# Kernel tuning notes

Hardware: AMD Instinct MI355X
Metric: run time of the kernel (lower is better)

Reference implementation:

```python
import jax, jax.numpy as jnp
import numpy as np
import math

STD = math.exp(0.0025)  # exp(0.5 * 0.005) from log_sigma = 0.005
C = 0.5 * math.log(2 * math.pi)
B, X, H, Z, L, W = 8192, 512, 256, 64, 16, 32

def _predict(h, Wd, bd, Wo, bo):
    return jax.nn.sigmoid(jax.nn.relu(h @ Wd.T + bd) @ Wo.T + bo)

def _gru(xin, h, Wih, Whh, bih, bhh):
    gi = xin @ Wih.T + bih
    gh = h @ Whh.T + bhh
    ir, iz, inn = jnp.split(gi, 3, axis=1)
    hr, hz, hn = jnp.split(gh, 3, axis=1)
    r = jax.nn.sigmoid(ir + hr)
    zt = jax.nn.sigmoid(iz + hz)
    n = jnp.tanh(inn + r * hn)
    return (1.0 - zt) * n + zt * h

def setup_inputs():
    key = jax.random.key(0)
    ks = iter(jax.random.split(key, 40))
    def nrm(shape, s=0.05):
        return jax.random.normal(next(ks), shape, dtype=jnp.float32) * s
    return {
        "x": jax.random.uniform(next(ks), (B, X), dtype=jnp.float32),
        "workers": jax.random.uniform(next(ks), (W, B, L), dtype=jnp.float32),
        "Wf1": nrm((H, X)), "bf1": jnp.zeros((H,)),
        "Wf2": nrm((1, H)), "bf2": jnp.zeros((1,)),
        "eWih": nrm((L, 3 * H, X + 1)), "eWhh": nrm((L, 3 * H, H)),
        "ebih": jnp.zeros((L, 3 * H)), "ebhh": jnp.zeros((L, 3 * H)),
        "eWd": nrm((L, H, H)), "ebd": jnp.zeros((L, H)),
        "eWo": nrm((L, 1, H)), "ebo": jnp.zeros((L, 1)),
        "Wmu": nrm((Z, H)), "bmu": jnp.zeros((Z,)),
        "Wlv": nrm((Z, H)), "blv": jnp.zeros((Z,)),
        "dWih": nrm((L, 3 * H, Z + 1)), "dWhh": nrm((L, 3 * H, H)),
        "dbih": jnp.zeros((L, 3 * H)), "dbhh": jnp.zeros((L, 3 * H)),
        "dWd": nrm((L, H, H)), "dbd": jnp.zeros((L, H)),
        "dWo": nrm((L, W, H)), "dbo": jnp.zeros((L, W)),
        "Wr": nrm((X, H)), "br": jnp.zeros((X,)),
        "enc_eps": jax.random.normal(next(ks), (L, B, H), dtype=jnp.float32),
        "samp_eps": jax.random.normal(next(ks), (B, Z), dtype=jnp.float32),
        "dec_eps": jax.random.uniform(next(ks), (L, B, H), dtype=jnp.float32),
    }

def _forward(x, workers, Wf1, bf1, Wf2, bf2, eWih, eWhh, ebih, ebhh, eWd, ebd, eWo, ebo,
             Wmu, bmu, Wlv, blv, dWih, dWhh, dbih, dbhh, dWd, dbd, dWo, dbo, Wr, br,
             enc_eps, samp_eps, dec_eps):
    nB = x.shape[0]
    h_dim = eWhh.shape[2]
    # Encoder: t[:,0] = firstcell(x)
    t0 = _predict(x, Wf1, bf1, Wf2, bf2)[:, 0]
    z0 = jnp.zeros((nB, h_dim), dtype=x.dtype)

    def enc_step(carry, xs):
        z, ti = carry
        Wih, Whh, bih, bhh, Wd, bd, Wo, bo, eps = xs
        tmp = (ti >= 0.5).astype(x.dtype)
        mu = _gru(jnp.concatenate([x, tmp[:, None]], axis=1), z, Wih, Whh, bih, bhh)
        znew = mu + STD * eps
        tn = _predict(znew, Wd, bd, Wo, bo)[:, 0]
        return (znew, tn), ti

    (z_fin, _), tcols = jax.lax.scan(
        enc_step, (z0, t0), (eWih, eWhh, ebih, ebhh, eWd, ebd, eWo, ebo, enc_eps))
    t = tcols.T  # [B, L]
    mu_z = z_fin @ Wmu.T + bmu
    log_var = jax.nn.softplus(z_fin @ Wlv.T + blv)
    latent = mu_z + jnp.exp(0.5 * log_var) * samp_eps
    tmp_t = (t > 0.5).astype(x.dtype)

    def dec_step(zt, xs):
        Wih, Whh, bih, bhh, Wd, bd, Wo, bo, tcol, eps = xs
        mu = _gru(jnp.concatenate([latent, tcol[:, None]], axis=1), zt, Wih, Whh, bih, bhh)
        znew = mu + STD * eps  # decoder uses uniform eps (torch.rand)
        return znew, _predict(znew, Wd, bd, Wo, bo)

    zT, preds = jax.lax.scan(
        dec_step, jnp.zeros((nB, h_dim), dtype=x.dtype),
        (dWih, dWhh, dbih, dbhh, dWd, dbd, dWo, dbo, tmp_t.T, dec_eps))
    worker_preds = jnp.transpose(preds, (2, 1, 0))  # [L,B,W] -> [W,B,L]
    recon = jax.nn.sigmoid(zT @ Wr.T + br)
    log_p_x = jnp.sum(x * jnp.log(recon), axis=1)
    logp = jnp.clip(jnp.log(worker_preds), -100.0)
    log1mp = jnp.clip(jnp.log1p(-worker_preds), -100.0)
    bce = -(workers * logp + (1.0 - workers) * log1mp)
    log_p_y = -jnp.sum(jnp.sum(bce, axis=0), axis=1)
    workers_bar = jnp.mean(workers, axis=0)
    log_kl = jnp.sum(t * (jnp.log(t + 1e-6) - jnp.log(workers_bar + 1e-6)), axis=1)
    log_p_z = jnp.sum(-C - latent ** 2 / 2, axis=-1)
    log_q = jnp.sum(-C - log_var / 2 - (latent - mu_z) ** 2 / (2 * jnp.exp(log_var)), axis=-1)
    loss = jnp.mean(log_q - log_p_z - log_p_y - log_p_x + log_kl)
    return t, loss

def reference(x, workers, Wf1, bf1, Wf2, bf2, eWih, eWhh, ebih, ebhh, eWd, ebd, eWo, ebo,
              Wmu, bmu, Wlv, blv, dWih, dWhh, dbih, dbhh, dWd, dbd, dWo, dbo, Wr, br,
              enc_eps, samp_eps, dec_eps):
    return _forward(x, workers, Wf1, bf1, Wf2, bf2, eWih, eWhh, ebih, ebhh, eWd, ebd,
                    eWo, ebo, Wmu, bmu, Wlv, blv, dWih, dWhh, dbih, dbhh, dWd, dbd,
                    dWo, dbo, Wr, br, enc_eps, samp_eps, dec_eps)
```

## Files before the change

kernel.cpp:

```cpp
#include <hip/hip_runtime.h>
#include <hip/hip_bf16.h>
#include <math.h>

#define B_ 8192
#define X_ 512
#define H_ 256
#define Z_ 64
#define L_ 16
#define W_ 32
#define G3_ 768

#define STDF 1.0025031276057952f
#define CC 0.9189385332046727f

typedef _Float16 f16x8 __attribute__((ext_vector_type(8)));
typedef float f32x4 __attribute__((ext_vector_type(4)));

__device__ __forceinline__ float sigm(float x) { return 1.0f / (1.0f + expf(-x)); }
__device__ __forceinline__ float logsig(float u) {
    return (u > 0.0f) ? -log1pf(expf(-u)) : (u - log1pf(expf(u)));
}

#define GLOAD16(gsrc, ldst) \
    __builtin_amdgcn_global_load_lds((const __attribute__((address_space(1))) unsigned int*)(gsrc), \
                                     (__attribute__((address_space(3))) unsigned int*)(ldst), 16, 0, 0)

#define WAITV(N) asm volatile("s_waitcnt vmcnt(" #N ")" ::: "memory")
#define SBAR()  do { __builtin_amdgcn_sched_barrier(0); __builtin_amdgcn_s_barrier(); } while (0)

template<int BN>
__global__ __launch_bounds__(256) void mfma_gemm(
    const _Float16* __restrict__ A,
    const _Float16* __restrict__ Wt,
    const float* __restrict__ bias,
    float* __restrict__ C, int ldc,
    int K, int act)
{
    constexpr int BM = 128;
    constexpr int WN = BN / 2;
    constexpr int NFR = WN / 16;
    __shared__ char smem[2][(BM + BN) * 128];

    const int tid  = threadIdx.x;
    const int wave = tid >> 6;
    const int lane = tid & 63;
    const int wr   = wave >> 1;
    const int wc   = wave & 1;
    const int bm   = blockIdx.y * BM;
    const int bn   = blockIdx.x * BN;
    const int l15  = lane & 15;
    const int l4   = lane >> 4;

    f32x4 acc[4][NFR];
    #pragma unroll
    for (int a = 0; a < 4; ++a)
        #pragma unroll
        for (int b = 0; b < NFR; ++b) {
            f32x4 zz = {0.f, 0.f, 0.f, 0.f};
            acc[a][b] = zz;
        }

    auto stage = [&](int s, int pb) {
        char* As = smem[pb];
        char* Ws = smem[pb] + BM * 128;
        int k0 = s * 64;
        #pragma unroll
        for (int it = 0; it < 4; ++it) {
            int q   = it * 4 + wave;
            int o   = q * 1024 + lane * 16;
            int row = o >> 7;
            int c   = ((o >> 4) & 7) ^ (row & 7);
            GLOAD16(A + (long)(bm + row) * K + k0 + c * 8, As + q * 1024);
        }
        #pragma unroll
        for (int it = 0; it < BN / 32; ++it) {
            int q   = it * 4 + wave;
            int o   = q * 1024 + lane * 16;
            int row = o >> 7;
            int c   = ((o >> 4) & 7) ^ (row & 7);
            GLOAD16(Wt + (long)(bn + row) * K + k0 + c * 8, Ws + q * 1024);
        }
    };

    const int NT = K >> 6;
    stage(0, 0);
    for (int s = 0; s < NT; ++s) {
        int pb = s & 1;
        if (s + 1 < NT) {
            stage(s + 1, pb ^ 1);
            if constexpr (BN == 128) WAITV(8); else WAITV(6);
        } else WAITV(0);
        SBAR();
        char* As = smem[pb];
        char* Ws = smem[pb] + BM * 128;
        #pragma unroll
        for (int ks = 0; ks < 2; ++ks) {
            f16x8 af[4], bf[NFR];
            #pragma unroll
            for (int mi = 0; mi < 4; ++mi) {
                int row = wr * 64 + mi * 16 + l15;
                int c   = (ks * 4 + l4) ^ (row & 7);
                af[mi] = *(const f16x8*)(As + row * 128 + c * 16);
            }
            #pragma unroll
            for (int ni = 0; ni < NFR; ++ni) {
                int row = wc * WN + ni * 16 + l15;
                int c   = (ks * 4 + l4) ^ (row & 7);
                bf[ni] = *(const f16x8*)(Ws + row * 128 + c * 16);
            }
            #pragma unroll
            for (int mi = 0; mi < 4; ++mi)
                #pragma unroll
                for (int ni = 0; ni < NFR; ++ni)
                    acc[mi][ni] = __builtin_amdgcn_mfma_f32_16x16x32_f16(
                        af[mi], bf[ni], acc[mi][ni], 0, 0, 0);
        }
        SBAR();
    }

    #pragma unroll
    for (int mi = 0; mi < 4; ++mi)
        #pragma unroll
        for (int r = 0; r < 4; ++r) {
            int grow = bm + wr * 64 + mi * 16 + l4 * 4 + r;
            #pragma unroll
            for (int ni = 0; ni < NFR; ++ni) {
                int gcol = bn + wc * WN + ni * 16 + l15;
                float v = acc[mi][ni][r] + bias[gcol];
                if (act) v = fmaxf(v, 0.0f);
                C[(long)grow * ldc + gcol] = v;
            }
        }
}

template<int MODE, int KX, int FIRST>
__global__ __launch_bounds__(256) void gru_fused(
    const _Float16* __restrict__ A2,
    const _Float16* __restrict__ Wih,
    const float* __restrict__ bih,
    const _Float16* __restrict__ Whh,
    const float* __restrict__ bhh,
    const float* __restrict__ ec,
    const float* __restrict__ tcol,
    const float* __restrict__ eps,
    const _Float16* __restrict__ zh_in,
    float* __restrict__ z,
    _Float16* __restrict__ zh_out)
{
    constexpr int N1 = KX / 64;
    constexpr int NT = N1 + (FIRST ? 0 : 4);
    __shared__ char smem[2][(64 + 192) * 128];

    const int tid  = threadIdx.x;
    const int wave = tid >> 6;
    const int lane = tid & 63;
    const int wr   = wave >> 1;
    const int wc   = wave & 1;
    const int id   = blockIdx.x;
    const int xcd  = id & 7;
    const int wk   = id >> 3;
    const int bm   = (xcd * 16 + (wk >> 2)) * 64;
    const int h0   = (wk & 3) * 64;
    const int l15  = lane & 15;
    const int l4   = lane >> 4;

    f32x4 acc[2][6];
    f32x4 accN[2][2];
    #pragma unroll
    for (int a = 0; a < 2; ++a) {
        #pragma unroll
        for (int b = 0; b < 6; ++b) { f32x4 zz = {0.f,0.f,0.f,0.f}; acc[a][b] = zz; }
        #pragma unroll
        for (int b = 0; b < 2; ++b) { f32x4 zz = {0.f,0.f,0.f,0.f}; accN[a][b] = zz; }
    }

    auto stage = [&](int s, int pb) {
        char* As = smem[pb];
        char* Ws = smem[pb] + 64 * 128;
        const _Float16* srcA;
        const _Float16* srcW;
        int KA, k0;
        if (s < N1) { srcA = A2;    srcW = Wih; KA = KX;  k0 = s * 64; }
        else        { srcA = zh_in; srcW = Whh; KA = 256; k0 = (s - N1) * 64; }
        #pragma unroll
        for (int it = 0; it < 2; ++it) {
            int q   = it * 4 + wave;
            int o   = q * 1024 + lane * 16;
            int row = o >> 7;
            int c   = ((o >> 4) & 7) ^ (row & 7);
            GLOAD16(srcA + (long)(bm + row) * KA + k0 + c * 8, As + q * 1024);
        }
        #pragma unroll
        for (int it = 0; it < 6; ++it) {
            int q   = it * 4 + wave;
            int o   = q * 1024 + lane * 16;
            int rr  = o >> 7;
            int c   = ((o >> 4) & 7) ^ (rr & 7);
            int srow = (rr >> 6) * 256 + h0 + (rr & 63);
            GLOAD16(srcW + (long)srow * KA + k0 + c * 8, Ws + q * 1024);
        }
    };

    stage(0, 0);
    for (int s = 0; s < NT; ++s) {
        int pb = s & 1;
        if (s + 1 < NT) { stage(s + 1, pb ^ 1); WAITV(8); }
        else WAITV(0);
        SBAR();
        char* As = smem[pb];
        char* Ws = smem[pb] + 64 * 128;
        bool p1 = (s < N1);
        #pragma unroll
        for (int ks = 0; ks < 2; ++ks) {
            f16x8 af[2], bf[6];
            #pragma unroll
            for (int mi = 0; mi < 2; ++mi) {
                int row = wr * 32 + mi * 16 + l15;
                int c   = (ks * 4 + l4) ^ (row & 7);
                af[mi] = *(const f16x8*)(As + row * 128 + c * 16);
            }
            #pragma unroll
            for (int ni = 0; ni < 6; ++ni) {
                int rr = (ni >> 1) * 64 + wc * 32 + (ni & 1) * 16 + l15;
                int c  = (ks * 4 + l4) ^ (rr & 7);
                bf[ni] = *(const f16x8*)(Ws + rr * 128 + c * 16);
            }
            if (p1) {
                #pragma unroll
                for (int mi = 0; mi < 2; ++mi) {
                    #pragma unroll
                    for (int ni = 0; ni < 4; ++ni)
                        acc[mi][ni] = __builtin_amdgcn_mfma_f32_16x16x32_f16(
                            af[mi], bf[ni], acc[mi][ni], 0, 0, 0);
                    #pragma unroll
                    for (int ni = 4; ni < 6; ++ni)
                        accN[mi][ni - 4] = __builtin_amdgcn_mfma_f32_16x16x32_f16(
                            af[mi], bf[ni], accN[mi][ni - 4], 0, 0, 0);
                }
            } else {
                #pragma unroll
                for (int mi = 0; mi < 2; ++mi)
                    #pragma unroll
                    for (int ni = 0; ni < 6; ++ni)
                        acc[mi][ni] = __builtin_amdgcn_mfma_f32_16x16x32_f16(
                            af[mi], bf[ni], acc[mi][ni], 0, 0, 0);
            }
        }
        SBAR();
    }

    #pragma unroll
    for (int mi = 0; mi < 2; ++mi)
        #pragma unroll
        for (int r = 0; r < 4; ++r) {
            int grow = bm + wr * 32 + mi * 16 + l4 * 4 + r;
            float tv = tcol[(long)grow * L_];
            float ext = (MODE == 1) ? (tv >= 0.5f ? 1.0f : 0.0f)
                                    : (tv >  0.5f ? 1.0f : 0.0f);
            #pragma unroll
            for (int hb = 0; hb < 2; ++hb) {
                int h = h0 + wc * 32 + hb * 16 + l15;
                float rpre = acc[mi][hb][r]     + bih[h]       + bhh[h]       + ext * ec[h];
                float zpre = acc[mi][2 + hb][r] + bih[256 + h] + bhh[256 + h] + ext * ec[256 + h];
                float hn   = acc[mi][4 + hb][r] + bhh[512 + h];
                float in_  = accN[mi][hb][r]    + bih[512 + h] + ext * ec[512 + h];
                float rg = sigm(rpre);
                float zt = sigm(zpre);
                float n  = tanhf(in_ + rg * hn);
                long zi = (long)grow * 256 + h;
                float zold = FIRST ? 0.0f : z[zi];
                float v = (1.0f - zt) * n + zt * zold + STDF * eps[zi];
                z[zi] = v;
                zh_out[zi] = (_Float16)v;
            }
        }
}

template<int K>
__global__ __launch_bounds__(256) void predict_head(
    const _Float16* __restrict__ A,
    const _Float16* __restrict__ Wd,
    const float* __restrict__ bd,
    const float* __restrict__ wo,
    const float* __restrict__ bo,
    float* __restrict__ out, int ostride)
{
    constexpr int NT = K / 64;
    __shared__ char smem[2][(32 + 256) * 128];
    __shared__ float part[32][4];

    const int tid  = threadIdx.x;
    const int wave = tid >> 6;
    const int lane = tid & 63;
    const int bm   = blockIdx.x * 32;
    const int l15  = lane & 15;
    const int l4   = lane >> 4;

    f32x4 acc[2][4];
    #pragma unroll
    for (int a = 0; a < 2; ++a)
        #pragma unroll
        for (int b = 0; b < 4; ++b) { f32x4 zz = {0.f,0.f,0.f,0.f}; acc[a][b] = zz; }

    auto stage = [&](int s, int pb) {
        char* As = smem[pb];
        char* Ws = smem[pb] + 32 * 128;
        int k0 = s * 64;
        {
            int o   = wave * 1024 + lane * 16;
            int row = o >> 7;
            int c   = ((o >> 4) & 7) ^ (row & 7);
            GLOAD16(A + (long)(bm + row) * K + k0 + c * 8, As + wave * 1024);
        }
        #pragma unroll
        for (int it = 0; it < 8; ++it) {
            int q   = it * 4 + wave;
            int o   = q * 1024 + lane * 16;
            int row = o >> 7;
            int c   = ((o >> 4) & 7) ^ (row & 7);
            GLOAD16(Wd + (long)row * K + k0 + c * 8, Ws + q * 1024);
        }
    };

    stage(0, 0);
    for (int s = 0; s < NT; ++s) {
        int pb = s & 1;
        if (s + 1 < NT) { stage(s + 1, pb ^ 1); WAITV(9); }
        else WAITV(0);
        SBAR();
        char* As = smem[pb];
        char* Ws = smem[pb] + 32 * 128;
        #pragma unroll
        for (int ks = 0; ks < 2; ++ks) {
            f16x8 af[2], bf[4];
            #pragma unroll
            for (int mi = 0; mi < 2; ++mi) {
                int row = mi * 16 + l15;
                int c   = (ks * 4 + l4) ^ (row & 7);
                af[mi] = *(const f16x8*)(As + row * 128 + c * 16);
            }
            #pragma unroll
            for (int ni = 0; ni < 4; ++ni) {
                int row = wave * 64 + ni * 16 + l15;
                int c   = (ks * 4 + l4) ^ (row & 7);
                bf[ni] = *(const f16x8*)(Ws + row * 128 + c * 16);
            }
            #pragma unroll
            for (int mi = 0; mi < 2; ++mi)
                #pragma unroll
                for (int ni = 0; ni < 4; ++ni)
                    acc[mi][ni] = __builtin_amdgcn_mfma_f32_16x16x32_f16(
                        af[mi], bf[ni], acc[mi][ni], 0, 0, 0);
        }
        SBAR();
    }

    float bdv[4], wov[4];
    #pragma unroll
    for (int ni = 0; ni < 4; ++ni) {
        int col = wave * 64 + ni * 16 + l15;
        bdv[ni] = bd[col];
        wov[ni] = wo[col];
    }
    #pragma unroll
    for (int mi = 0; mi < 2; ++mi)
        #pragma unroll
        for (int r = 0; r < 4; ++r) {
            float s = 0.0f;
            #pragma unroll
            for (int ni = 0; ni < 4; ++ni) {
                float v = fmaxf(acc[mi][ni][r] + bdv[ni], 0.0f);
                s = fmaf(v, wov[ni], s);
            }
            #pragma unroll
            for (int off = 1; off < 16; off <<= 1) s += __shfl_xor(s, off, 16);
            if (l15 == 0) part[mi * 16 + l4 * 4 + r][wave] = s;
        }
    __syncthreads();
    if (tid < 32) {
        float u = part[tid][0] + part[tid][1] + part[tid][2] + part[tid][3] + bo[0];
        out[(long)(bm + tid) * ostride] = sigm(u);
    }
}

__global__ __launch_bounds__(256) void dec_head_bce(
    const _Float16* __restrict__ A,
    const _Float16* __restrict__ Wd,
    const float* __restrict__ bd,
    const _Float16* __restrict__ Wo,
    const float* __restrict__ bo,
    const float* __restrict__ wt,
    float* __restrict__ bacc)
{
    constexpr int NT = 4;
    __shared__ char smem[2][(32 + 256) * 128];
    __shared__ _Float16 ds[32 * 264];
    __shared__ float part[32][2];

    const int tid  = threadIdx.x;
    const int wave = tid >> 6;
    const int lane = tid & 63;
    const int bm   = blockIdx.x * 32;
    const int l15  = lane & 15;
    const int l4   = lane >> 4;

    f32x4 acc[2][4];
    #pragma unroll
    for (int a = 0; a < 2; ++a)
        #pragma unroll
        for (int b = 0; b < 4; ++b) { f32x4 zz = {0.f,0.f,0.f,0.f}; acc[a][b] = zz; }

    auto stage = [&](int s, int pb) {
        char* As = smem[pb];
        char* Ws = smem[pb] + 32 * 128;
        int k0 = s * 64;
        {
            int o   = wave * 1024 + lane * 16;
            int row = o >> 7;
            int c   = ((o >> 4) & 7) ^ (row & 7);
            GLOAD16(A + (long)(bm + row) * 256 + k0 + c * 8, As + wave * 1024);
        }
        #pragma unroll
        for (int it = 0; it < 8; ++it) {
            int q   = it * 4 + wave;
            int o   = q * 1024 + lane * 16;
            int row = o >> 7;
            int c   = ((o >> 4) & 7) ^ (row & 7);
            GLOAD16(Wd + (long)row * 256 + k0 + c * 8, Ws + q * 1024);
        }
    };

    stage(0, 0);
    for (int s = 0; s < NT; ++s) {
        int pb = s & 1;
        if (s + 1 < NT) { stage(s + 1, pb ^ 1); WAITV(9); }
        else WAITV(0);
        SBAR();
        char* As = smem[pb];
        char* Ws = smem[pb] + 32 * 128;
        #pragma unroll
        for (int ks = 0; ks < 2; ++ks) {
            f16x8 af[2], bf[4];
            #pragma unroll
            for (int mi = 0; mi < 2; ++mi) {
                int row = mi * 16 + l15;
                int c   = (ks * 4 + l4) ^ (row & 7);
                af[mi] = *(const f16x8*)(As + row * 128 + c * 16);
            }
            #pragma unroll
            for (int ni = 0; ni < 4; ++ni) {
                int row = wave * 64 + ni * 16 + l15;
                int c   = (ks * 4 + l4) ^ (row & 7);
                bf[ni] = *(const f16x8*)(Ws + row * 128 + c * 16);
            }
            #pragma unroll
            for (int mi = 0; mi < 2; ++mi)
                #pragma unroll
                for (int ni = 0; ni < 4; ++ni)
                    acc[mi][ni] = __builtin_amdgcn_mfma_f32_16x16x32_f16(
                        af[mi], bf[ni], acc[mi][ni], 0, 0, 0);
        }
        SBAR();
    }

    #pragma unroll
    for (int mi = 0; mi < 2; ++mi)
        #pragma unroll
        for (int r = 0; r < 4; ++r) {
            int row = mi * 16 + l4 * 4 + r;
            #pragma unroll
            for (int ni = 0; ni < 4; ++ni) {
                int col = wave * 64 + ni * 16 + l15;
                ds[row * 264 + col] = (_Float16)fmaxf(acc[mi][ni][r] + bd[col], 0.0f);
            }
        }
    __syncthreads();

    const int rh = wave >> 1;
    const int ch = wave & 1;
    f32x4 acc2 = {0.f, 0.f, 0.f, 0.f};
    #pragma unroll
    for (int k = 0; k < 8; ++k) {
        f16x8 bf2 = *(const f16x8*)(Wo + (long)(ch * 16 + l15) * 256 + k * 32 + l4 * 8);
        f16x8 af  = *(const f16x8*)(ds + (rh * 16 + l15) * 264 + k * 32 + l4 * 8);
        acc2 = __builtin_amdgcn_mfma_f32_16x16x32_f16(af, bf2, acc2, 0, 0, 0);
    }

    #pragma unroll
    for (int r = 0; r < 4; ++r) {
        int row = rh * 16 + l4 * 4 + r;
        int w = ch * 16 + l15;
        float u = acc2[r] + bo[w];
        float logp   = fmaxf(logsig(u),  -100.0f);
        float log1mp = fmaxf(logsig(-u), -100.0f);
        float wk = wt[(long)(bm + row) * W_ + w];
        float s = -(wk * logp + (1.0f - wk) * log1mp);
        #pragma unroll
        for (int off = 1; off < 16; off <<= 1) s += __shfl_xor(s, off, 16);
        if (l15 == 0) part[row][ch] = s;
    }
    __syncthreads();
    if (tid < 32) bacc[bm + tid] += part[tid][0] + part[tid][1];
}

__global__ __launch_bounds__(256) void wtrans(
    const float* __restrict__ workers, float* __restrict__ wt,
    float* __restrict__ bacc)
{
    long idx = (long)blockIdx.x * 256 + threadIdx.x;
    int w = idx & 31;
    long b = idx >> 5;
    const float* src = workers + (w * (long)B_ + b) * L_;
    #pragma unroll
    for (int l = 0; l < L_; ++l)
        wt[((long)l * B_ + b) * W_ + w] = src[l];
    if (w == 0) bacc[b] = 0.0f;
}

struct ConvJobs {
    const float* s[10];
    _Float16* d[10];
};
__device__ __constant__ const long CJ_CNT[10] = {
    (long)B_ * X_,
    (long)H_ * X_,
    (long)L_ * G3_ * H_,
    (long)L_ * H_ * H_,
    (long)L_ * G3_ * H_,
    (long)L_ * H_ * H_,
    (long)L_ * W_ * H_,
    (long)X_ * H_,
    (long)Z_ * H_,
    (long)Z_ * H_
};
#define CJ_TOTAL 13008896L

__global__ __launch_bounds__(256) void conv_multi(ConvJobs J)
{
    long i8 = ((long)blockIdx.x * 256 + threadIdx.x) * 8;
    if (i8 >= CJ_TOTAL) return;
    long rem = i8; int j = 0;
    #pragma unroll
    for (int k = 0; k < 9; ++k)
        if (rem >= CJ_CNT[k]) { rem -= CJ_CNT[k]; ++j; } else break;
    const float* s = J.s[j] + rem;
    f16x8 o;
    #pragma unroll
    for (int q = 0; q < 8; ++q) o[q] = (_Float16)s[q];
    *(f16x8*)(J.d[j] + rem) = o;
}

__global__ __launch_bounds__(256) void conv_f16(
    const float* __restrict__ src, _Float16* __restrict__ dst,
    int Ks, int Kd, long total)
{
    long i = ((long)blockIdx.x * 256 + threadIdx.x) * 8;
    if (i >= total) return;
    long r = i / Kd, k = i - r * Kd;
    const float* s = src + r * Ks + k;
    f16x8 o;
    #pragma unroll
    for (int j = 0; j < 8; ++j) o[j] = (_Float16)s[j];
    *(f16x8*)(dst + i) = o;
}

__global__ __launch_bounds__(256) void extract_col(
    const float* __restrict__ src, float* __restrict__ dst, int Ks, int col, int R)
{
    int i = blockIdx.x * 256 + threadIdx.x;
    if (i < R) dst[i] = src[(long)i * Ks + col];
}

__global__ void stack_bias(const float* __restrict__ a, const float* __restrict__ b,
                           float* __restrict__ o)
{
    int i = threadIdx.x;
    o[i] = (i < 64) ? a[i] : b[i - 64];
}

__global__ __launch_bounds__(256) void latent_elem(
    const float* __restrict__ muv,
    const float* __restrict__ seps,
    float* __restrict__ latent, _Float16* __restrict__ lath,
    float* __restrict__ lq, float* __restrict__ lpz)
{
    int wave = threadIdx.x >> 6, lane = threadIdx.x & 63;
    int b = blockIdx.x * 4 + wave;
    float mu = muv[(long)b * 128 + lane];
    float sp = muv[(long)b * 128 + 64 + lane];
    float lv = (sp > 0.0f) ? (sp + log1pf(expf(-sp))) : log1pf(expf(sp));
    float e  = seps[(long)b * Z_ + lane];
    float lat = mu + expf(0.5f * lv) * e;
    latent[(long)b * Z_ + lane] = lat;
    lath[(long)b * Z_ + lane] = (_Float16)lat;
    float lpz_c = -CC - 0.5f * lat * lat;
    float d = lat - mu;
    float lq_c = -CC - 0.5f * lv - d * d / (2.0f * expf(lv));
    #pragma unroll
    for (int off = 32; off; off >>= 1) {
        lpz_c += __shfl_down(lpz_c, off);
        lq_c  += __shfl_down(lq_c, off);
    }
    if (lane == 0) { lpz[b] = lpz_c; lq[b] = lq_c; }
}

__global__ __launch_bounds__(256) void logpx_reduce(
    const float* __restrict__ u, const float* __restrict__ x,
    float* __restrict__ lpx)
{
    int wave = threadIdx.x >> 6, lane = threadIdx.x & 63;
    int b = blockIdx.x * 4 + wave;
    const float* ub = u + (long)b * X_;
    const float* xb = x + (long)b * X_;
    float s = 0.0f;
    #pragma unroll
    for (int i = 0; i < 8; ++i) {
        int k = lane + i * 64;
        s = fmaf(xb[k], logsig(ub[k]), s);
    }
    #pragma unroll
    for (int off = 32; off; off >>= 1) s += __shfl_down(s, off);
    if (lane == 0) lpx[b] = s;
}

__global__ __launch_bounds__(256) void kl_kernel(
    const float* __restrict__ tmat, const float* __restrict__ workers,
    float* __restrict__ lkl)
{
    int b = blockIdx.x * 256 + threadIdx.x;
    float wb[L_];
    #pragma unroll
    for (int l = 0; l < L_; ++l) wb[l] = 0.0f;
    for (int w = 0; w < W_; ++w) {
        const float* p = workers + ((long)w * B_ + b) * L_;
        #pragma unroll
        for (int l = 0; l < L_; ++l) wb[l] += p[l];
    }
    float s = 0.0f;
    #pragma unroll
    for (int l = 0; l < L_; ++l) {
        float wbar = wb[l] * (1.0f / 32.0f);
        float tv = tmat[(long)b * L_ + l];
        s += tv * (logf(tv + 1e-6f) - logf(wbar + 1e-6f));
    }
    lkl[b] = s;
}

__global__ __launch_bounds__(1024) void final_reduce(
    const float* __restrict__ lq, const float* __restrict__ lpz,
    const float* __restrict__ bacc, const float* __restrict__ lpx,
    const float* __restrict__ lkl, float* __restrict__ out)
{
    __shared__ float red[16];
    float s = 0.0f;
    for (int b = threadIdx.x; b < B_; b += 1024)
        s += lq[b] - lpz[b] + bacc[b] - lpx[b] + lkl[b];
    #pragma unroll
    for (int off = 32; off; off >>= 1) s += __shfl_down(s, off);
    int wave = threadIdx.x >> 6, lane = threadIdx.x & 63;
    if (lane == 0) red[wave] = s;
    __syncthreads();
    if (threadIdx.x == 0) {
        float t = 0.0f;
        for (int i = 0; i < 16; ++i) t += red[i];
        out[0] = t / (float)B_;
    }
}

extern "C" void kernel_launch(void* const* d_in, const int* in_sizes, int n_in,
                              void* d_out, int out_size, void* d_ws, size_t ws_size,
                              hipStream_t stream)
{
    const float* x       = (const float*)d_in[0];
    const float* workers = (const float*)d_in[1];
    const float* Wf1     = (const float*)d_in[2];
    const float* bf1     = (const float*)d_in[3];
    const float* Wf2     = (const float*)d_in[4];
    const float* bf2     = (const float*)d_in[5];
    const float* eWih    = (const float*)d_in[6];
    const float* eWhh    = (const float*)d_in[7];
    const float* ebih    = (const float*)d_in[8];
    const float* ebhh    = (const float*)d_in[9];
    const float* eWd     = (const float*)d_in[10];
    const float* ebd     = (const float*)d_in[11];
    const float* eWo     = (const float*)d_in[12];
    const float* ebo     = (const float*)d_in[13];
    const float* Wmu     = (const float*)d_in[14];
    const float* bmu     = (const float*)d_in[15];
    const float* Wlv     = (const float*)d_in[16];
    const float* blv     = (const float*)d_in[17];
    const float* dWih    = (const float*)d_in[18];
    const float* dWhh    = (const float*)d_in[19];
    const float* dbih    = (const float*)d_in[20];
    const float* dbhh    = (const float*)d_in[21];
    const float* dWd     = (const float*)d_in[22];
    const float* dbd     = (const float*)d_in[23];
    const float* dWo     = (const float*)d_in[24];
    const float* dbo     = (const float*)d_in[25];
    const float* Wr      = (const float*)d_in[26];
    const float* br      = (const float*)d_in[27];
    const float* enc_eps = (const float*)d_in[28];
    const float* samp_eps= (const float*)d_in[29];
    const float* dec_eps = (const float*)d_in[30];

    float* t    = (float*)d_out;
    float* loss = t + (long)B_ * L_;

    char* p = (char*)d_ws;
    auto alloc = [&](size_t bytes) {
        char* r = p;
        p += (bytes + 255) & ~(size_t)255;
        return r;
    };
    _Float16* xh    = (_Float16*)alloc((size_t)B_ * X_ * 2);
    _Float16* zha   = (_Float16*)alloc((size_t)B_ * H_ * 2);
    _Float16* zhb   = (_Float16*)alloc((size_t)B_ * H_ * 2);
    _Float16* lath  = (_Float16*)alloc((size_t)B_ * Z_ * 2);
    _Float16* Wf1h  = (_Float16*)alloc((size_t)H_ * X_ * 2);
    _Float16* eWihh = (_Float16*)alloc((size_t)L_ * G3_ * X_ * 2);
    _Float16* eWhhh = (_Float16*)alloc((size_t)L_ * G3_ * H_ * 2);
    _Float16* eWdh  = (_Float16*)alloc((size_t)L_ * H_ * H_ * 2);
    _Float16* dWihh = (_Float16*)alloc((size_t)L_ * G3_ * Z_ * 2);
    _Float16* dWhhh = (_Float16*)alloc((size_t)L_ * G3_ * H_ * 2);
    _Float16* dWdh  = (_Float16*)alloc((size_t)L_ * H_ * H_ * 2);
    _Float16* dWoh  = (_Float16*)alloc((size_t)L_ * W_ * H_ * 2);
    _Float16* Wrh   = (_Float16*)alloc((size_t)X_ * H_ * 2);
    _Float16* Wmlh  = (_Float16*)alloc((size_t)128 * H_ * 2);
    float* bml    = (float*)alloc(128 * 4);
    float* eWihc  = (float*)alloc((size_t)L_ * G3_ * 4);
    float* dWihc  = (float*)alloc((size_t)L_ * G3_ * 4);
    float* z      = (float*)alloc((size_t)B_ * H_ * 4);
    float* dbuf   = (float*)alloc((size_t)B_ * H_ * 4);
    float* latent = (float*)alloc((size_t)B_ * Z_ * 4);
    float* wt     = (float*)alloc((size_t)L_ * B_ * W_ * 4);
    float* logits = (float*)alloc((size_t)B_ * X_ * 4);
    float* lq     = (float*)alloc((size_t)B_ * 4);
    float* lpz    = (float*)alloc((size_t)B_ * 4);
    float* lpx    = (float*)alloc((size_t)B_ * 4);
    float* lkl    = (float*)alloc((size_t)B_ * 4);
    float* bacc   = (float*)alloc((size_t)B_ * 4);

    const dim3 blk(256);
    const int nBH = B_ * H_;
    auto cgrid = [](long total) { return dim3((unsigned)((total / 8 + 255) / 256)); };

    ConvJobs J;
    J.s[0] = x;    J.d[0] = xh;
    J.s[1] = Wf1;  J.d[1] = Wf1h;
    J.s[2] = eWhh; J.d[2] = eWhhh;
    J.s[3] = eWd;  J.d[3] = eWdh;
    J.s[4] = dWhh; J.d[4] = dWhhh;
    J.s[5] = dWd;  J.d[5] = dWdh;
    J.s[6] = dWo;  J.d[6] = dWoh;
    J.s[7] = Wr;   J.d[7] = Wrh;
    J.s[8] = Wmu;  J.d[8] = Wmlh;
    J.s[9] = Wlv;  J.d[9] = Wmlh + (long)Z_ * H_;
    conv_multi<<<(CJ_TOTAL / 8 + 255) / 256, blk, 0, stream>>>(J);
    conv_f16<<<cgrid((long)L_ * G3_ * X_), blk, 0, stream>>>(eWih, eWihh, X_ + 1, X_, (long)L_ * G3_ * X_);
    conv_f16<<<cgrid((long)L_ * G3_ * Z_), blk, 0, stream>>>(dWih, dWihh, Z_ + 1, Z_, (long)L_ * G3_ * Z_);
    stack_bias<<<1, 128, 0, stream>>>(bmu, blv, bml);
    extract_col<<<(L_ * G3_ + 255) / 256, blk, 0, stream>>>(eWih, eWihc, X_ + 1, X_, L_ * G3_);
    extract_col<<<(L_ * G3_ + 255) / 256, blk, 0, stream>>>(dWih, dWihc, Z_ + 1, Z_, L_ * G3_);
    wtrans<<<(W_ * B_) / 256, blk, 0, stream>>>(workers, wt, bacc);

    predict_head<X_><<<B_ / 32, blk, 0, stream>>>(xh, Wf1h, bf1, Wf2, bf2, t, L_);

    _Float16* zcur = zha;
    _Float16* znxt = zhb;
    for (int l = 0; l < L_; ++l) {
        if (l == 0)
            gru_fused<1, X_, 1><<<512, blk, 0, stream>>>(
                xh, eWihh, ebih, eWhhh, ebhh, eWihc, t, enc_eps, zcur, z, znxt);
        else
            gru_fused<1, X_, 0><<<512, blk, 0, stream>>>(
                xh, eWihh + (long)l * G3_ * X_, ebih + (long)l * G3_,
                eWhhh + (long)l * G3_ * H_, ebhh + (long)l * G3_,
                eWihc + (long)l * G3_, t + l, enc_eps + (long)l * nBH,
                zcur, z, znxt);
        _Float16* tmp = zcur; zcur = znxt; znxt = tmp;
        if (l < L_ - 1)
            predict_head<H_><<<B_ / 32, blk, 0, stream>>>(
                zcur, eWdh + (long)l * H_ * H_, ebd + (long)l * H_,
                eWo + (long)l * H_, ebo + l, t + (l + 1), L_);
    }

    mfma_gemm<64><<<dim3(2, B_ / 128), blk, 0, stream>>>(
        zcur, Wmlh, bml, dbuf, 128, H_, 0);
    latent_elem<<<B_ / 4, blk, 0, stream>>>(dbuf, samp_eps, latent, lath, lq, lpz);

    zcur = zha; znxt = zhb;
    for (int l = 0; l < L_; ++l) {
        if (l == 0)
            gru_fused<2, Z_, 1><<<512, blk, 0, stream>>>(
                lath, dWihh, dbih, dWhhh, dbhh, dWihc, t, dec_eps, zcur, z, znxt);
        else
            gru_fused<2, Z_, 0><<<512, blk, 0, stream>>>(
                lath, dWihh + (long)l * G3_ * Z_, dbih + (long)l * G3_,
                dWhhh + (long)l * G3_ * H_, dbhh + (long)l * G3_,
                dWihc + (long)l * G3_, t + l, dec_eps + (long)l * nBH,
                zcur, z, znxt);
        _Float16* tmp = zcur; zcur = znxt; znxt = tmp;
        dec_head_bce<<<B_ / 32, blk, 0, stream>>>(
            zcur, dWdh + (long)l * H_ * H_, dbd + (long)l * H_,
            dWoh + (long)l * W_ * H_, dbo + (long)l * W_,
            wt + (long)l * B_ * W_, bacc);
    }

    mfma_gemm<128><<<dim3(X_ / 128, B_ / 128), blk, 0, stream>>>(
        zcur, Wrh, br, logits, X_, H_, 0);
    logpx_reduce<<<B_ / 4, blk, 0, stream>>>(logits, x, lpx);
    kl_kernel<<<B_ / 256, blk, 0, stream>>>(t, workers, lkl);
    final_reduce<<<1, 1024, 0, stream>>>(lq, lpz, bacc, lpx, lkl, loss);
}
```

Measured before the change: 1.107 ms.

## Fuse encoder and decoder scans into persistent cooperative kernels with grid sync

Replaces roughly seventy per-step kernel launches (GRU steps, predict heads, latent, BCE heads, reconstruction, reductions) with two cooperative persistent kernels of 256 blocks by 512 threads. Each phase (GRU, head, latent, BCE, logpx, KL, final reduce) becomes a device function, and grid-wide barriers sit between the dependent steps. GRU tiles grow to 128 rows, and the heads split their N dimension across 8 waves. This removes launch gaps and intermediate buffers such as the logits and mu/logvar arrays, at the cost of grid-sync overhead and a limit of one large block per CU that may reduce occupancy.

```diff
diff --git a/kernel.cpp b/kernel.cpp
--- a/kernel.cpp
+++ b/kernel.cpp
@@ -1,6 +1,9 @@
 #include <hip/hip_runtime.h>
 #include <hip/hip_bf16.h>
+#include <hip/hip_cooperative_groups.h>
 #include <math.h>
+
+namespace cg = cooperative_groups;
 
 #define B_ 8192
 #define X_ 512
@@ -26,130 +29,20 @@
                                      (__attribute__((address_space(3))) unsigned int*)(ldst), 16, 0, 0)
 
 #define WAITV(N) asm volatile("s_waitcnt vmcnt(" #N ")" ::: "memory")
+#define WAITV0() asm volatile("s_waitcnt vmcnt(0)" ::: "memory")
 #define SBAR()  do { __builtin_amdgcn_sched_barrier(0); __builtin_amdgcn_s_barrier(); } while (0)
 
-template<int BN>
-__global__ __launch_bounds__(256) void mfma_gemm(
-    const _Float16* __restrict__ A,
-    const _Float16* __restrict__ Wt,
-    const float* __restrict__ bias,
-    float* __restrict__ C, int ldc,
-    int K, int act)
-{
-    constexpr int BM = 128;
-    constexpr int WN = BN / 2;
-    constexpr int NFR = WN / 16;
-    __shared__ char smem[2][(BM + BN) * 128];
-
-    const int tid  = threadIdx.x;
-    const int wave = tid >> 6;
-    const int lane = tid & 63;
-    const int wr   = wave >> 1;
-    const int wc   = wave & 1;
-    const int bm   = blockIdx.y * BM;
-    const int bn   = blockIdx.x * BN;
-    const int l15  = lane & 15;
-    const int l4   = lane >> 4;
-
-    f32x4 acc[4][NFR];
-    #pragma unroll
-    for (int a = 0; a < 4; ++a)
-        #pragma unroll
-        for (int b = 0; b < NFR; ++b) {
-            f32x4 zz = {0.f, 0.f, 0.f, 0.f};
-            acc[a][b] = zz;
-        }
-
-    auto stage = [&](int s, int pb) {
-        char* As = smem[pb];
-        char* Ws = smem[pb] + BM * 128;
-        int k0 = s * 64;
-        #pragma unroll
-        for (int it = 0; it < 4; ++it) {
-            int q   = it * 4 + wave;
-            int o   = q * 1024 + lane * 16;
-            int row = o >> 7;
-            int c   = ((o >> 4) & 7) ^ (row & 7);
-            GLOAD16(A + (long)(bm + row) * K + k0 + c * 8, As + q * 1024);
-        }
-        #pragma unroll
-        for (int it = 0; it < BN / 32; ++it) {
-            int q   = it * 4 + wave;
-            int o   = q * 1024 + lane * 16;
-            int row = o >> 7;
-            int c   = ((o >> 4) & 7) ^ (row & 7);
-            GLOAD16(Wt + (long)(bn + row) * K + k0 + c * 8, Ws + q * 1024);
-        }
-    };
-
-    const int NT = K >> 6;
-    stage(0, 0);
-    for (int s = 0; s < NT; ++s) {
-        int pb = s & 1;
-        if (s + 1 < NT) {
-            stage(s + 1, pb ^ 1);
-            if constexpr (BN == 128) WAITV(8); else WAITV(6);
-        } else WAITV(0);
-        SBAR();
-        char* As = smem[pb];
-        char* Ws = smem[pb] + BM * 128;
-        #pragma unroll
-        for (int ks = 0; ks < 2; ++ks) {
-            f16x8 af[4], bf[NFR];
-            #pragma unroll
-            for (int mi = 0; mi < 4; ++mi) {
-                int row = wr * 64 + mi * 16 + l15;
-                int c   = (ks * 4 + l4) ^ (row & 7);
-                af[mi] = *(const f16x8*)(As + row * 128 + c * 16);
-            }
-            #pragma unroll
-            for (int ni = 0; ni < NFR; ++ni) {
-                int row = wc * WN + ni * 16 + l15;
-                int c   = (ks * 4 + l4) ^ (row & 7);
-                bf[ni] = *(const f16x8*)(Ws + row * 128 + c * 16);
-            }
-            #pragma unroll
-            for (int mi = 0; mi < 4; ++mi)
-                #pragma unroll
-                for (int ni = 0; ni < NFR; ++ni)
-                    acc[mi][ni] = __builtin_amdgcn_mfma_f32_16x16x32_f16(
-                        af[mi], bf[ni], acc[mi][ni], 0, 0, 0);
-        }
-        SBAR();
-    }
-
-    #pragma unroll
-    for (int mi = 0; mi < 4; ++mi)
-        #pragma unroll
-        for (int r = 0; r < 4; ++r) {
-            int grow = bm + wr * 64 + mi * 16 + l4 * 4 + r;
-            #pragma unroll
-            for (int ni = 0; ni < NFR; ++ni) {
-                int gcol = bn + wc * WN + ni * 16 + l15;
-                float v = acc[mi][ni][r] + bias[gcol];
-                if (act) v = fmaxf(v, 0.0f);
-                C[(long)grow * ldc + gcol] = v;
-            }
-        }
-}
-
-template<int MODE, int KX, int FIRST>
-__global__ __launch_bounds__(256) void gru_fused(
-    const _Float16* __restrict__ A2,
-    const _Float16* __restrict__ Wih,
-    const float* __restrict__ bih,
-    const _Float16* __restrict__ Whh,
-    const float* __restrict__ bhh,
-    const float* __restrict__ ec,
-    const float* __restrict__ tcol,
-    const float* __restrict__ eps,
-    const _Float16* __restrict__ zh_in,
-    float* __restrict__ z,
-    _Float16* __restrict__ zh_out)
+template<int MODE, int KX>
+__device__ void gru_phase(char (*smem)[40960],
+    const _Float16* __restrict__ A2, const _Float16* __restrict__ Wih,
+    const float* __restrict__ bih, const _Float16* __restrict__ Whh,
+    const float* __restrict__ bhh, const float* __restrict__ ec,
+    const float* __restrict__ tcol, const float* __restrict__ eps,
+    const _Float16* __restrict__ zh_in, float* __restrict__ z,
+    _Float16* __restrict__ zh_out, bool first)
 {
     constexpr int N1 = KX / 64;
-    constexpr int NT = N1 + (FIRST ? 0 : 4);
-    __shared__ char smem[2][(64 + 192) * 128];
+    const int NT = N1 + (first ? 0 : 4);
 
     const int tid  = threadIdx.x;
     const int wave = tid >> 6;
@@ -159,7 +52,7 @@
     const int id   = blockIdx.x;
     const int xcd  = id & 7;
     const int wk   = id >> 3;
-    const int bm   = (xcd * 16 + (wk >> 2)) * 64;
+    const int bm   = (xcd * 8 + (wk >> 2)) * 128;
     const int h0   = (wk & 3) * 64;
     const int l15  = lane & 15;
     const int l4   = lane >> 4;
@@ -176,39 +69,37 @@
 
     auto stage = [&](int s, int pb) {
         char* As = smem[pb];
-        char* Ws = smem[pb] + 64 * 128;
+        char* Ws = smem[pb] + 16384;
         const _Float16* srcA;
         const _Float16* srcW;
         int KA, k0;
         if (s < N1) { srcA = A2;    srcW = Wih; KA = KX;  k0 = s * 64; }
         else        { srcA = zh_in; srcW = Whh; KA = 256; k0 = (s - N1) * 64; }
         #pragma unroll
-        for (int it = 0; it < 2; ++it) {
-            int q   = it * 4 + wave;
-            int o   = q * 1024 + lane * 16;
-            int row = o >> 7;
-            int c   = ((o >> 4) & 7) ^ (row & 7);
-            GLOAD16(srcA + (long)(bm + row) * KA + k0 + c * 8, As + q * 1024);
-        }
-        #pragma unroll
-        for (int it = 0; it < 6; ++it) {
-            int q   = it * 4 + wave;
-            int o   = q * 1024 + lane * 16;
-            int rr  = o >> 7;
-            int c   = ((o >> 4) & 7) ^ (rr & 7);
+        for (int q = 0; q < 2; ++q) {
+            int f   = q * 8192 + tid * 16;
+            int row = f >> 7;
+            int c   = ((f >> 4) & 7) ^ (row & 7);
+            GLOAD16(srcA + (long)(bm + row) * KA + k0 + c * 8, As + f);
+        }
+        #pragma unroll
+        for (int q = 0; q < 3; ++q) {
+            int f   = q * 8192 + tid * 16;
+            int rr  = f >> 7;
+            int c   = ((f >> 4) & 7) ^ (rr & 7);
             int srow = (rr >> 6) * 256 + h0 + (rr & 63);
-            GLOAD16(srcW + (long)srow * KA + k0 + c * 8, Ws + q * 1024);
+            GLOAD16(srcW + (long)srow * KA + k0 + c * 8, Ws + f);
         }
     };
 
     stage(0, 0);
     for (int s = 0; s < NT; ++s) {
         int pb = s & 1;
-        if (s + 1 < NT) { stage(s + 1, pb ^ 1); WAITV(8); }
-        else WAITV(0);
-        SBAR();
-        char* As = smem[pb];
-        char* Ws = smem[pb] + 64 * 128;
+        if (s + 1 < NT) { stage(s + 1, pb ^ 1); WAITV(5); }
+        else WAITV0();
+        SBAR();
+        char* As = smem[pb];
+        char* Ws = smem[pb] + 16384;
         bool p1 = (s < N1);
         #pragma unroll
         for (int ks = 0; ks < 2; ++ks) {
@@ -268,57 +159,52 @@
                 float zt = sigm(zpre);
                 float n  = tanhf(in_ + rg * hn);
                 long zi = (long)grow * 256 + h;
-                float zold = FIRST ? 0.0f : z[zi];
+                float zold = first ? 0.0f : z[zi];
                 float v = (1.0f - zt) * n + zt * zold + STDF * eps[zi];
                 z[zi] = v;
                 zh_out[zi] = (_Float16)v;
             }
         }
-}
-
-template<int K>
-__global__ __launch_bounds__(256) void predict_head(
-    const _Float16* __restrict__ A,
-    const _Float16* __restrict__ Wd,
-    const float* __restrict__ bd,
-    const float* __restrict__ wo,
-    const float* __restrict__ bo,
+    WAITV0();
+}
+
+__device__ void predict_phase(char (*smem)[40960], float* part,
+    const _Float16* __restrict__ A, int K,
+    const _Float16* __restrict__ Wd, const float* __restrict__ bd,
+    const float* __restrict__ wo, const float* __restrict__ bo,
     float* __restrict__ out, int ostride)
 {
-    constexpr int NT = K / 64;
-    __shared__ char smem[2][(32 + 256) * 128];
-    __shared__ float part[32][4];
-
+    const int NT = K >> 6;
     const int tid  = threadIdx.x;
     const int wave = tid >> 6;
     const int lane = tid & 63;
-    const int bm   = blockIdx.x * 32;
+    const int bm2  = blockIdx.x * 32;
     const int l15  = lane & 15;
     const int l4   = lane >> 4;
 
-    f32x4 acc[2][4];
+    f32x4 acc[2][2];
     #pragma unroll
     for (int a = 0; a < 2; ++a)
         #pragma unroll
-        for (int b = 0; b < 4; ++b) { f32x4 zz = {0.f,0.f,0.f,0.f}; acc[a][b] = zz; }
+        for (int b = 0; b < 2; ++b) { f32x4 zz = {0.f,0.f,0.f,0.f}; acc[a][b] = zz; }
 
     auto stage = [&](int s, int pb) {
         char* As = smem[pb];
-        char* Ws = smem[pb] + 32 * 128;
-        int k0 = s * 64;
-        {
-            int o   = wave * 1024 + lane * 16;
-            int row = o >> 7;
-            int c   = ((o >> 4) & 7) ^ (row & 7);
-            GLOAD16(A + (long)(bm + row) * K + k0 + c * 8, As + wave * 1024);
-        }
-        #pragma unroll
-        for (int it = 0; it < 8; ++it) {
-            int q   = it * 4 + wave;
-            int o   = q * 1024 + lane * 16;
-            int row = o >> 7;
-            int c   = ((o >> 4) & 7) ^ (row & 7);
-            GLOAD16(Wd + (long)row * K + k0 + c * 8, Ws + q * 1024);
+        char* Ws = smem[pb] + 4096;
+        if (tid < 256) {
+            {
+                int f   = tid * 16;
+                int row = f >> 7;
+                int c   = ((f >> 4) & 7) ^ (row & 7);
+                GLOAD16(A + (long)(bm2 + row) * K + s * 64 + c * 8, As + f);
+            }
+            #pragma unroll
+            for (int q = 0; q < 8; ++q) {
+                int f   = q * 4096 + tid * 16;
+                int row = f >> 7;
+                int c   = ((f >> 4) & 7) ^ (row & 7);
+                GLOAD16(Wd + (long)row * K + s * 64 + c * 8, Ws + f);
+            }
         }
     };
 
@@ -326,13 +212,13 @@
     for (int s = 0; s < NT; ++s) {
         int pb = s & 1;
         if (s + 1 < NT) { stage(s + 1, pb ^ 1); WAITV(9); }
-        else WAITV(0);
-        SBAR();
-        char* As = smem[pb];
-        char* Ws = smem[pb] + 32 * 128;
+        else WAITV0();
+        SBAR();
+        char* As = smem[pb];
+        char* Ws = smem[pb] + 4096;
         #pragma unroll
         for (int ks = 0; ks < 2; ++ks) {
-            f16x8 af[2], bf[4];
+            f16x8 af[2], bf[2];
             #pragma unroll
             for (int mi = 0; mi < 2; ++mi) {
                 int row = mi * 16 + l15;
@@ -340,8 +226,333 @@
                 af[mi] = *(const f16x8*)(As + row * 128 + c * 16);
             }
             #pragma unroll
+            for (int ni = 0; ni < 2; ++ni) {
+                int row = wave * 32 + ni * 16 + l15;
+                int c   = (ks * 4 + l4) ^ (row & 7);
+                bf[ni] = *(const f16x8*)(Ws + row * 128 + c * 16);
+            }
+            #pragma unroll
+            for (int mi = 0; mi < 2; ++mi)
+                #pragma unroll
+                for (int ni = 0; ni < 2; ++ni)
+                    acc[mi][ni] = __builtin_amdgcn_mfma_f32_16x16x32_f16(
+                        af[mi], bf[ni], acc[mi][ni], 0, 0, 0);
+        }
+        SBAR();
+    }
+
+    float bdv[2], wov[2];
+    #pragma unroll
+    for (int ni = 0; ni < 2; ++ni) {
+        int col = wave * 32 + ni * 16 + l15;
+        bdv[ni] = bd[col];
+        wov[ni] = wo[col];
+    }
+    #pragma unroll
+    for (int mi = 0; mi < 2; ++mi)
+        #pragma unroll
+        for (int r = 0; r < 4; ++r) {
+            float s = 0.0f;
+            #pragma unroll
+            for (int ni = 0; ni < 2; ++ni) {
+                float v = fmaxf(acc[mi][ni][r] + bdv[ni], 0.0f);
+                s = fmaf(v, wov[ni], s);
+            }
+            #pragma unroll
+            for (int off = 1; off < 16; off <<= 1) s += __shfl_xor(s, off, 16);
+            if (l15 == 0) part[(mi * 16 + l4 * 4 + r) * 8 + wave] = s;
+        }
+    __syncthreads();
+    if (tid < 32) {
+        float u = bo[0];
+        #pragma unroll
+        for (int w = 0; w < 8; ++w) u += part[tid * 8 + w];
+        out[(long)(bm2 + tid) * ostride] = sigm(u);
+    }
+    __syncthreads();
+    WAITV0();
+}
+
+__device__ void latent_phase(char (*smem)[40960], float* muv ,
+    const _Float16* __restrict__ A, const _Float16* __restrict__ Wml,
+    const float* __restrict__ bml, const float* __restrict__ seps,
+    _Float16* __restrict__ lath, float* __restrict__ lq, float* __restrict__ lpz)
+{
+    const int tid  = threadIdx.x;
+    const int wave = tid >> 6;
+    const int lane = tid & 63;
+    const int bm2  = blockIdx.x * 32;
+    const int l15  = lane & 15;
+    const int l4   = lane >> 4;
+
+    f32x4 acc[2];
+    { f32x4 zz = {0.f,0.f,0.f,0.f}; acc[0] = zz; acc[1] = zz; }
+
+    auto stage = [&](int s, int pb) {
+        char* As = smem[pb];
+        char* Ws = smem[pb] + 4096;
+        if (tid < 256) {
+            {
+                int f   = tid * 16;
+                int row = f >> 7;
+                int c   = ((f >> 4) & 7) ^ (row & 7);
+                GLOAD16(A + (long)(bm2 + row) * 256 + s * 64 + c * 8, As + f);
+            }
+            #pragma unroll
+            for (int q = 0; q < 4; ++q) {
+                int f   = q * 4096 + tid * 16;
+                int row = f >> 7;
+                int c   = ((f >> 4) & 7) ^ (row & 7);
+                GLOAD16(Wml + (long)row * 256 + s * 64 + c * 8, Ws + f);
+            }
+        }
+    };
+
+    stage(0, 0);
+    for (int s = 0; s < 4; ++s) {
+        int pb = s & 1;
+        if (s + 1 < 4) { stage(s + 1, pb ^ 1); WAITV(5); }
+        else WAITV0();
+        SBAR();
+        char* As = smem[pb];
+        char* Ws = smem[pb] + 4096;
+        #pragma unroll
+        for (int ks = 0; ks < 2; ++ks) {
+            f16x8 af[2], bf;
+            #pragma unroll
+            for (int mi = 0; mi < 2; ++mi) {
+                int row = mi * 16 + l15;
+                int c   = (ks * 4 + l4) ^ (row & 7);
+                af[mi] = *(const f16x8*)(As + row * 128 + c * 16);
+            }
+            {
+                int row = wave * 16 + l15;
+                int c   = (ks * 4 + l4) ^ (row & 7);
+                bf = *(const f16x8*)(Ws + row * 128 + c * 16);
+            }
+            #pragma unroll
+            for (int mi = 0; mi < 2; ++mi)
+                acc[mi] = __builtin_amdgcn_mfma_f32_16x16x32_f16(af[mi], bf, acc[mi], 0, 0, 0);
+        }
+        SBAR();
+    }
+
+    #pragma unroll
+    for (int mi = 0; mi < 2; ++mi)
+        #pragma unroll
+        for (int r = 0; r < 4; ++r) {
+            int row = mi * 16 + l4 * 4 + r;
+            int col = wave * 16 + l15;
+            muv[row * 132 + col] = acc[mi][r] + bml[col];
+        }
+    __syncthreads();
+
+    int row = tid >> 4;
+    int g   = tid & 15;
+    float lpz_c = 0.0f, lq_c = 0.0f;
+    #pragma unroll
+    for (int j = 0; j < 4; ++j) {
+        int zc = g * 4 + j;
+        float mu = muv[row * 132 + zc];
+        float sp = muv[row * 132 + 64 + zc];
+        float lv = (sp > 0.0f) ? (sp + log1pf(expf(-sp))) : log1pf(expf(sp));
+        float e  = seps[(long)(bm2 + row) * Z_ + zc];
+        float lat = mu + expf(0.5f * lv) * e;
+        lath[(long)(bm2 + row) * Z_ + zc] = (_Float16)lat;
+        lpz_c += -CC - 0.5f * lat * lat;
+        float d = lat - mu;
+        lq_c += -CC - 0.5f * lv - d * d / (2.0f * expf(lv));
+    }
+    #pragma unroll
+    for (int off = 1; off < 16; off <<= 1) {
+        lpz_c += __shfl_xor(lpz_c, off, 16);
+        lq_c  += __shfl_xor(lq_c, off, 16);
+    }
+    if (g == 0) { lpz[bm2 + row] = lpz_c; lq[bm2 + row] = lq_c; }
+    __syncthreads();
+    WAITV0();
+}
+
+__device__ void bce_phase(char (*smem)[40960], char* aux,
+    const _Float16* __restrict__ A, const _Float16* __restrict__ Wd,
+    const float* __restrict__ bd, const _Float16* __restrict__ Wo,
+    const float* __restrict__ bo, const float* __restrict__ wtl,
+    float* __restrict__ bacc)
+{
+    _Float16* ds = (_Float16*)aux;
+    float* part  = (float*)(aux + 16896);
+
+    const int tid  = threadIdx.x;
+    const int wave = tid >> 6;
+    const int lane = tid & 63;
+    const int bm2  = blockIdx.x * 32;
+    const int l15  = lane & 15;
+    const int l4   = lane >> 4;
+
+    f32x4 acc[2][2];
+    #pragma unroll
+    for (int a = 0; a < 2; ++a)
+        #pragma unroll
+        for (int b = 0; b < 2; ++b) { f32x4 zz = {0.f,0.f,0.f,0.f}; acc[a][b] = zz; }
+
+    auto stage = [&](int s, int pb) {
+        char* As = smem[pb];
+        char* Ws = smem[pb] + 4096;
+        if (tid < 256) {
+            {
+                int f   = tid * 16;
+                int row = f >> 7;
+                int c   = ((f >> 4) & 7) ^ (row & 7);
+                GLOAD16(A + (long)(bm2 + row) * 256 + s * 64 + c * 8, As + f);
+            }
+            #pragma unroll
+            for (int q = 0; q < 8; ++q) {
+                int f   = q * 4096 + tid * 16;
+                int row = f >> 7;
+                int c   = ((f >> 4) & 7) ^ (row & 7);
+                GLOAD16(Wd + (long)row * 256 + s * 64 + c * 8, Ws + f);
+            }
+        }
+    };
+
+    stage(0, 0);
+    for (int s = 0; s < 4; ++s) {
+        int pb = s & 1;
+        if (s + 1 < 4) { stage(s + 1, pb ^ 1); WAITV(9); }
+        else WAITV0();
+        SBAR();
+        char* As = smem[pb];
+        char* Ws = smem[pb] + 4096;
+        #pragma unroll
+        for (int ks = 0; ks < 2; ++ks) {
+            f16x8 af[2], bf[2];
+            #pragma unroll
+            for (int mi = 0; mi < 2; ++mi) {
+                int row = mi * 16 + l15;
+                int c   = (ks * 4 + l4) ^ (row & 7);
+                af[mi] = *(const f16x8*)(As + row * 128 + c * 16);
+            }
+            #pragma unroll
+            for (int ni = 0; ni < 2; ++ni) {
+                int row = wave * 32 + ni * 16 + l15;
+                int c   = (ks * 4 + l4) ^ (row & 7);
+                bf[ni] = *(const f16x8*)(Ws + row * 128 + c * 16);
+            }
+            #pragma unroll
+            for (int mi = 0; mi < 2; ++mi)
+                #pragma unroll
+                for (int ni = 0; ni < 2; ++ni)
+                    acc[mi][ni] = __builtin_amdgcn_mfma_f32_16x16x32_f16(
+                        af[mi], bf[ni], acc[mi][ni], 0, 0, 0);
+        }
+        SBAR();
+    }
+
+    #pragma unroll
+    for (int mi = 0; mi < 2; ++mi)
+        #pragma unroll
+        for (int r = 0; r < 4; ++r) {
+            int row = mi * 16 + l4 * 4 + r;
+            #pragma unroll
+            for (int ni = 0; ni < 2; ++ni) {
+                int col = wave * 32 + ni * 16 + l15;
+                ds[row * 264 + col] = (_Float16)fmaxf(acc[mi][ni][r] + bd[col], 0.0f);
+            }
+        }
+    __syncthreads();
+
+    if (wave < 4) {
+        const int rh = wave >> 1;
+        const int ch = wave & 1;
+        f32x4 acc2 = {0.f, 0.f, 0.f, 0.f};
+        #pragma unroll
+        for (int k = 0; k < 8; ++k) {
+            f16x8 bf2 = *(const f16x8*)(Wo + (long)(ch * 16 + l15) * 256 + k * 32 + l4 * 8);
+            f16x8 af  = *(const f16x8*)(ds + (rh * 16 + l15) * 264 + k * 32 + l4 * 8);
+            acc2 = __builtin_amdgcn_mfma_f32_16x16x32_f16(af, bf2, acc2, 0, 0, 0);
+        }
+        #pragma unroll
+        for (int r = 0; r < 4; ++r) {
+            int row = rh * 16 + l4 * 4 + r;
+            int w = ch * 16 + l15;
+            float u = acc2[r] + bo[w];
+            float logp   = fmaxf(logsig(u),  -100.0f);
+            float log1mp = fmaxf(logsig(-u), -100.0f);
+            float wk = wtl[(long)(bm2 + row) * W_ + w];
+            float s = -(wk * logp + (1.0f - wk) * log1mp);
+            #pragma unroll
+            for (int off = 1; off < 16; off <<= 1) s += __shfl_xor(s, off, 16);
+            if (l15 == 0) part[row * 2 + ch] = s;
+        }
+    }
+    __syncthreads();
+    if (tid < 32) bacc[bm2 + tid] += part[tid * 2 + 0] + part[tid * 2 + 1];
+    __syncthreads();
+    WAITV0();
+}
+
+__device__ void recon_phase(char (*smem)[40960], char* aux,
+    const _Float16* __restrict__ A, const _Float16* __restrict__ Wt,
+    const float* __restrict__ bias, const float* __restrict__ x,
+    float* __restrict__ lpx)
+{
+    float* part = (float*)aux;
+
+    const int tid  = threadIdx.x;
+    const int wave = tid >> 6;
+    const int lane = tid & 63;
+    const int wr   = wave >> 1;
+    const int wc   = wave & 1;
+    const int bm   = (blockIdx.x >> 2) * 128;
+    const int bn   = (blockIdx.x & 3) * 128;
+    const int l15  = lane & 15;
+    const int l4   = lane >> 4;
+
+    f32x4 acc[2][4];
+    #pragma unroll
+    for (int a = 0; a < 2; ++a)
+        #pragma unroll
+        for (int b = 0; b < 4; ++b) { f32x4 zz = {0.f,0.f,0.f,0.f}; acc[a][b] = zz; }
+
+    auto stage = [&](int s, int pb) {
+        char* As = smem[pb];
+        char* Ws = smem[pb] + 16384;
+        #pragma unroll
+        for (int q = 0; q < 2; ++q) {
+            int f   = q * 8192 + tid * 16;
+            int row = f >> 7;
+            int c   = ((f >> 4) & 7) ^ (row & 7);
+            GLOAD16(A + (long)(bm + row) * 256 + s * 64 + c * 8, As + f);
+        }
+        #pragma unroll
+        for (int q = 0; q < 2; ++q) {
+            int f   = q * 8192 + tid * 16;
+            int row = f >> 7;
+            int c   = ((f >> 4) & 7) ^ (row & 7);
+            GLOAD16(Wt + (long)(bn + row) * 256 + s * 64 + c * 8, Ws + f);
+        }
+    };
+
+    stage(0, 0);
+    for (int s = 0; s < 4; ++s) {
+        int pb = s & 1;
+        if (s + 1 < 4) { stage(s + 1, pb ^ 1); WAITV(4); }
+        else WAITV0();
+        SBAR();
+        char* As = smem[pb];
+        char* Ws = smem[pb] + 16384;
+        #pragma unroll
+        for (int ks = 0; ks < 2; ++ks) {
+            f16x8 af[2], bf[4];
+            #pragma unroll
+            for (int mi = 0; mi < 2; ++mi) {
+                int row = wr * 32 + mi * 16 + l15;
+                int c   = (ks * 4 + l4) ^ (row & 7);
+                af[mi] = *(const f16x8*)(As + row * 128 + c * 16);
+            }
+            #pragma unroll
             for (int ni = 0; ni < 4; ++ni) {
-                int row = wave * 64 + ni * 16 + l15;
+                int row = wc * 64 + ni * 16 + l15;
                 int c   = (ks * 4 + l4) ^ (row & 7);
                 bf[ni] = *(const f16x8*)(Ws + row * 128 + c * 16);
             }
@@ -355,157 +566,150 @@
         SBAR();
     }
 
-    float bdv[4], wov[4];
-    #pragma unroll
-    for (int ni = 0; ni < 4; ++ni) {
-        int col = wave * 64 + ni * 16 + l15;
-        bdv[ni] = bd[col];
-        wov[ni] = wo[col];
-    }
     #pragma unroll
     for (int mi = 0; mi < 2; ++mi)
         #pragma unroll
         for (int r = 0; r < 4; ++r) {
+            int grow = bm + wr * 32 + mi * 16 + l4 * 4 + r;
             float s = 0.0f;
             #pragma unroll
             for (int ni = 0; ni < 4; ++ni) {
-                float v = fmaxf(acc[mi][ni][r] + bdv[ni], 0.0f);
-                s = fmaf(v, wov[ni], s);
+                int gcol = bn + wc * 64 + ni * 16 + l15;
+                float u = acc[mi][ni][r] + bias[gcol];
+                s = fmaf(x[(long)grow * X_ + gcol], logsig(u), s);
             }
             #pragma unroll
             for (int off = 1; off < 16; off <<= 1) s += __shfl_xor(s, off, 16);
-            if (l15 == 0) part[mi * 16 + l4 * 4 + r][wave] = s;
-        }
-    __syncthreads();
-    if (tid < 32) {
-        float u = part[tid][0] + part[tid][1] + part[tid][2] + part[tid][3] + bo[0];
-        out[(long)(bm + tid) * ostride] = sigm(u);
-    }
-}
-
-__global__ __launch_bounds__(256) void dec_head_bce(
-    const _Float16* __restrict__ A,
-    const _Float16* __restrict__ Wd,
-    const float* __restrict__ bd,
-    const _Float16* __restrict__ Wo,
-    const float* __restrict__ bo,
-    const float* __restrict__ wt,
-    float* __restrict__ bacc)
-{
-    constexpr int NT = 4;
-    __shared__ char smem[2][(32 + 256) * 128];
-    __shared__ _Float16 ds[32 * 264];
-    __shared__ float part[32][2];
-
-    const int tid  = threadIdx.x;
-    const int wave = tid >> 6;
-    const int lane = tid & 63;
-    const int bm   = blockIdx.x * 32;
-    const int l15  = lane & 15;
-    const int l4   = lane >> 4;
-
-    f32x4 acc[2][4];
-    #pragma unroll
-    for (int a = 0; a < 2; ++a)
-        #pragma unroll
-        for (int b = 0; b < 4; ++b) { f32x4 zz = {0.f,0.f,0.f,0.f}; acc[a][b] = zz; }
-
-    auto stage = [&](int s, int pb) {
-        char* As = smem[pb];
-        char* Ws = smem[pb] + 32 * 128;
-        int k0 = s * 64;
-        {
-            int o   = wave * 1024 + lane * 16;
-            int row = o >> 7;
-            int c   = ((o >> 4) & 7) ^ (row & 7);
-            GLOAD16(A + (long)(bm + row) * 256 + k0 + c * 8, As + wave * 1024);
-        }
-        #pragma unroll
-        for (int it = 0; it < 8; ++it) {
-            int q   = it * 4 + wave;
-            int o   = q * 1024 + lane * 16;
-            int row = o >> 7;
-            int c   = ((o >> 4) & 7) ^ (row & 7);
-            GLOAD16(Wd + (long)row * 256 + k0 + c * 8, Ws + q * 1024);
-        }
-    };
-
-    stage(0, 0);
-    for (int s = 0; s < NT; ++s) {
-        int pb = s & 1;
-        if (s + 1 < NT) { stage(s + 1, pb ^ 1); WAITV(9); }
-        else WAITV(0);
-        SBAR();
-        char* As = smem[pb];
-        char* Ws = smem[pb] + 32 * 128;
-        #pragma unroll
-        for (int ks = 0; ks < 2; ++ks) {
-            f16x8 af[2], bf[4];
-            #pragma unroll
-            for (int mi = 0; mi < 2; ++mi) {
-                int row = mi * 16 + l15;
-                int c   = (ks * 4 + l4) ^ (row & 7);
-                af[mi] = *(const f16x8*)(As + row * 128 + c * 16);
-            }
-            #pragma unroll
-            for (int ni = 0; ni < 4; ++ni) {
-                int row = wave * 64 + ni * 16 + l15;
-                int c   = (ks * 4 + l4) ^ (row & 7);
-                bf[ni] = *(const f16x8*)(Ws + row * 128 + c * 16);
-            }
-            #pragma unroll
-            for (int mi = 0; mi < 2; ++mi)
-                #pragma unroll
-                for (int ni = 0; ni < 4; ++ni)
-                    acc[mi][ni] = __builtin_amdgcn_mfma_f32_16x16x32_f16(
-                        af[mi], bf[ni], acc[mi][ni], 0, 0, 0);
-        }
-        SBAR();
-    }
-
-    #pragma unroll
-    for (int mi = 0; mi < 2; ++mi)
-        #pragma unroll
-        for (int r = 0; r < 4; ++r) {
-            int row = mi * 16 + l4 * 4 + r;
-            #pragma unroll
-            for (int ni = 0; ni < 4; ++ni) {
-                int col = wave * 64 + ni * 16 + l15;
-                ds[row * 264 + col] = (_Float16)fmaxf(acc[mi][ni][r] + bd[col], 0.0f);
-            }
-        }
-    __syncthreads();
-
-    const int rh = wave >> 1;
-    const int ch = wave & 1;
-    f32x4 acc2 = {0.f, 0.f, 0.f, 0.f};
-    #pragma unroll
-    for (int k = 0; k < 8; ++k) {
-        f16x8 bf2 = *(const f16x8*)(Wo + (long)(ch * 16 + l15) * 256 + k * 32 + l4 * 8);
-        f16x8 af  = *(const f16x8*)(ds + (rh * 16 + l15) * 264 + k * 32 + l4 * 8);
-        acc2 = __builtin_amdgcn_mfma_f32_16x16x32_f16(af, bf2, acc2, 0, 0, 0);
-    }
-
-    #pragma unroll
-    for (int r = 0; r < 4; ++r) {
-        int row = rh * 16 + l4 * 4 + r;
-        int w = ch * 16 + l15;
-        float u = acc2[r] + bo[w];
-        float logp   = fmaxf(logsig(u),  -100.0f);
-        float log1mp = fmaxf(logsig(-u), -100.0f);
-        float wk = wt[(long)(bm + row) * W_ + w];
-        float s = -(wk * logp + (1.0f - wk) * log1mp);
-        #pragma unroll
-        for (int off = 1; off < 16; off <<= 1) s += __shfl_xor(s, off, 16);
-        if (l15 == 0) part[row][ch] = s;
-    }
-    __syncthreads();
-    if (tid < 32) bacc[bm + tid] += part[tid][0] + part[tid][1];
+            if (l15 == 0) part[(wr * 32 + mi * 16 + l4 * 4 + r) * 2 + wc] = s;
+        }
+    __syncthreads();
+    if (tid < 128) atomicAdd(&lpx[bm + tid], part[tid * 2] + part[tid * 2 + 1]);
+    __syncthreads();
+    WAITV0();
+}
+
+__device__ void kl_phase(const float* __restrict__ tmat,
+    const float* __restrict__ workers, float* __restrict__ lkl)
+{
+    if (threadIdx.x >= 32) return;
+    int b = blockIdx.x * 32 + threadIdx.x;
+    float wb[L_];
+    #pragma unroll
+    for (int l = 0; l < L_; ++l) wb[l] = 0.0f;
+    for (int w = 0; w < W_; ++w) {
+        const float* p = workers + (w * (long)B_ + b) * L_;
+        #pragma unroll
+        for (int l = 0; l < L_; ++l) wb[l] += p[l];
+    }
+    float s = 0.0f;
+    #pragma unroll
+    for (int l = 0; l < L_; ++l) {
+        float wbar = wb[l] * (1.0f / 32.0f);
+        float tv = tmat[(long)b * L_ + l];
+        s += tv * (logf(tv + 1e-6f) - logf(wbar + 1e-6f));
+    }
+    lkl[b] = s;
+}
+
+__device__ void final_phase(char* aux,
+    const float* __restrict__ lq, const float* __restrict__ lpz,
+    const float* __restrict__ bacc, const float* __restrict__ lpx,
+    const float* __restrict__ lkl, float* __restrict__ out)
+{
+    if (blockIdx.x != 0) return;
+    float* red = (float*)aux;
+    float s = 0.0f;
+    for (int b = threadIdx.x; b < B_; b += 512)
+        s += lq[b] - lpz[b] + bacc[b] - lpx[b] + lkl[b];
+    #pragma unroll
+    for (int off = 32; off; off >>= 1) s += __shfl_down(s, off);
+    int wave = threadIdx.x >> 6, lane = threadIdx.x & 63;
+    if (lane == 0) red[wave] = s;
+    __syncthreads();
+    if (threadIdx.x == 0) {
+        float t = 0.0f;
+        for (int i = 0; i < 8; ++i) t += red[i];
+        out[0] = t / (float)B_;
+    }
+}
+
+struct EncP {
+    const _Float16 *xh, *Wf1h, *eWihh, *eWhhh, *eWdh;
+    const float *bf1, *Wf2, *bf2, *ebih, *ebhh, *eWihc, *ebd, *eWo, *ebo;
+    const float *enc_eps, *workers;
+    float *t, *z, *lkl;
+    _Float16 *zb0, *zb1;
+};
+
+__global__ __launch_bounds__(512) void enc_scan(EncP P)
+{
+    __shared__ char smem[2][40960];
+    __shared__ char aux[17408];
+    cg::grid_group grid = cg::this_grid();
+
+    predict_phase(smem, (float*)aux, P.xh, X_, P.Wf1h, P.bf1, P.Wf2, P.bf2, P.t, L_);
+    grid.sync();
+    for (int l = 0; l < L_; ++l) {
+        const _Float16* zin  = (l & 1) ? P.zb1 : P.zb0;
+        _Float16*       zout = ((l + 1) & 1) ? P.zb1 : P.zb0;
+        gru_phase<1, X_>(smem, P.xh, P.eWihh + (long)l * G3_ * X_, P.ebih + l * G3_,
+                         P.eWhhh + (long)l * G3_ * H_, P.ebhh + l * G3_,
+                         P.eWihc + l * G3_, P.t + l, P.enc_eps + (long)l * B_ * H_,
+                         zin, P.z, zout, l == 0);
+        grid.sync();
+        if (l < L_ - 1) {
+            predict_phase(smem, (float*)aux, zout, H_,
+                          P.eWdh + (long)l * H_ * H_, P.ebd + l * H_,
+                          P.eWo + l * H_, P.ebo + l, P.t + (l + 1), L_);
+            grid.sync();
+        }
+    }
+    kl_phase(P.t, P.workers, P.lkl);
+}
+
+struct DecP {
+    const _Float16 *zfin, *Wmlh, *dWihh, *dWhhh, *dWdh, *dWoh, *Wrh;
+    const float *bml, *samp_eps, *dbih, *dbhh, *dWihc, *dbd, *dbo, *br, *x, *wtr;
+    const float *t, *dec_eps;
+    _Float16 *lath, *zb0, *zb1;
+    float *z, *lq, *lpz, *bacc, *lpx, *lkl, *loss;
+};
+
+__global__ __launch_bounds__(512) void dec_scan(DecP P)
+{
+    __shared__ char smem[2][40960];
+    __shared__ char aux[17408];
+    cg::grid_group grid = cg::this_grid();
+
+    latent_phase(smem, (float*)aux, P.zfin, P.Wmlh, P.bml, P.samp_eps,
+                 P.lath, P.lq, P.lpz);
+    grid.sync();
+    for (int l = 0; l < L_; ++l) {
+        const _Float16* zin  = (l & 1) ? P.zb1 : P.zb0;
+        _Float16*       zout = ((l + 1) & 1) ? P.zb1 : P.zb0;
+        gru_phase<2, Z_>(smem, P.lath, P.dWihh + (long)l * G3_ * Z_, P.dbih + l * G3_,
+                         P.dWhhh + (long)l * G3_ * H_, P.dbhh + l * G3_,
+                         P.dWihc + l * G3_, P.t + l, P.dec_eps + (long)l * B_ * H_,
+                         zin, P.z, zout, l == 0);
+        if (l > 0) {
+            const _Float16* zh = (l & 1) ? P.zb1 : P.zb0;
+            bce_phase(smem, aux, zh, P.dWdh + (long)(l - 1) * H_ * H_,
+                      P.dbd + (l - 1) * H_, P.dWoh + (long)(l - 1) * W_ * H_,
+                      P.dbo + (l - 1) * W_, P.wtr + (long)(l - 1) * B_ * W_, P.bacc);
+        }
+        grid.sync();
+    }
+    bce_phase(smem, aux, P.zb0, P.dWdh + (long)15 * H_ * H_, P.dbd + 15 * H_,
+              P.dWoh + (long)15 * W_ * H_, P.dbo + 15 * W_,
+              P.wtr + (long)15 * B_ * W_, P.bacc);
+    recon_phase(smem, aux, P.zb0, P.Wrh, P.br, P.x, P.lpx);
+    grid.sync();
+    final_phase(aux, P.lq, P.lpz, P.bacc, P.lpx, P.lkl, P.loss);
 }
 
 __global__ __launch_bounds__(256) void wtrans(
     const float* __restrict__ workers, float* __restrict__ wt,
-    float* __restrict__ bacc)
+    float* __restrict__ bacc, float* __restrict__ lpx)
 {
     long idx = (long)blockIdx.x * 256 + threadIdx.x;
     int w = idx & 31;
@@ -514,7 +718,7 @@
     #pragma unroll
     for (int l = 0; l < L_; ++l)
         wt[((long)l * B_ + b) * W_ + w] = src[l];
-    if (w == 0) bacc[b] = 0.0f;
+    if (w == 0) { bacc[b] = 0.0f; lpx[b] = 0.0f; }
 }
 
 struct ConvJobs {
@@ -522,16 +726,9 @@
     _Float16* d[10];
 };
 __device__ __constant__ const long CJ_CNT[10] = {
-    (long)B_ * X_,
-    (long)H_ * X_,
-    (long)L_ * G3_ * H_,
-    (long)L_ * H_ * H_,
-    (long)L_ * G3_ * H_,
-    (long)L_ * H_ * H_,
-    (long)L_ * W_ * H_,
-    (long)X_ * H_,
-    (long)Z_ * H_,
-    (long)Z_ * H_
+    (long)B_ * X_, (long)H_ * X_, (long)L_ * G3_ * H_, (long)L_ * H_ * H_,
+    (long)L_ * G3_ * H_, (long)L_ * H_ * H_, (long)L_ * W_ * H_,
+    (long)X_ * H_, (long)Z_ * H_, (long)Z_ * H_
 };
 #define CJ_TOTAL 13008896L
 
@@ -576,95 +773,6 @@
 {
     int i = threadIdx.x;
     o[i] = (i < 64) ? a[i] : b[i - 64];
-}
-
-__global__ __launch_bounds__(256) void latent_elem(
-    const float* __restrict__ muv,
-    const float* __restrict__ seps,
-    float* __restrict__ latent, _Float16* __restrict__ lath,
-    float* __restrict__ lq, float* __restrict__ lpz)
-{
-    int wave = threadIdx.x >> 6, lane = threadIdx.x & 63;
-    int b = blockIdx.x * 4 + wave;
-    float mu = muv[(long)b * 128 + lane];
-    float sp = muv[(long)b * 128 + 64 + lane];
-    float lv = (sp > 0.0f) ? (sp + log1pf(expf(-sp))) : log1pf(expf(sp));
-    float e  = seps[(long)b * Z_ + lane];
-    float lat = mu + expf(0.5f * lv) * e;
-    latent[(long)b * Z_ + lane] = lat;
-    lath[(long)b * Z_ + lane] = (_Float16)lat;
-    float lpz_c = -CC - 0.5f * lat * lat;
-    float d = lat - mu;
-    float lq_c = -CC - 0.5f * lv - d * d / (2.0f * expf(lv));
-    #pragma unroll
-    for (int off = 32; off; off >>= 1) {
-        lpz_c += __shfl_down(lpz_c, off);
-        lq_c  += __shfl_down(lq_c, off);
-    }
-    if (lane == 0) { lpz[b] = lpz_c; lq[b] = lq_c; }
-}
-
-__global__ __launch_bounds__(256) void logpx_reduce(
-    const float* __restrict__ u, const float* __restrict__ x,
-    float* __restrict__ lpx)
-{
-    int wave = threadIdx.x >> 6, lane = threadIdx.x & 63;
-    int b = blockIdx.x * 4 + wave;
-    const float* ub = u + (long)b * X_;
-    const float* xb = x + (long)b * X_;
-    float s = 0.0f;
-    #pragma unroll
-    for (int i = 0; i < 8; ++i) {
-        int k = lane + i * 64;
-        s = fmaf(xb[k], logsig(ub[k]), s);
-    }
-    #pragma unroll
-    for (int off = 32; off; off >>= 1) s += __shfl_down(s, off);
-    if (lane == 0) lpx[b] = s;
-}
-
-__global__ __launch_bounds__(256) void kl_kernel(
-    const float* __restrict__ tmat, const float* __restrict__ workers,
-    float* __restrict__ lkl)
-{
-    int b = blockIdx.x * 256 + threadIdx.x;
-    float wb[L_];
-    #pragma unroll
-    for (int l = 0; l < L_; ++l) wb[l] = 0.0f;
-    for (int w = 0; w < W_; ++w) {
-        const float* p = workers + ((long)w * B_ + b) * L_;
-        #pragma unroll
-        for (int l = 0; l < L_; ++l) wb[l] += p[l];
-    }
-    float s = 0.0f;
-    #pragma unroll
-    for (int l = 0; l < L_; ++l) {
-        float wbar = wb[l] * (1.0f / 32.0f);
-        float tv = tmat[(long)b * L_ + l];
-        s += tv * (logf(tv + 1e-6f) - logf(wbar + 1e-6f));
-    }
-    lkl[b] = s;
-}
-
-__global__ __launch_bounds__(1024) void final_reduce(
-    const float* __restrict__ lq, const float* __restrict__ lpz,
-    const float* __restrict__ bacc, const float* __restrict__ lpx,
-    const float* __restrict__ lkl, float* __restrict__ out)
-{
-    __shared__ float red[16];
-    float s = 0.0f;
-    for (int b = threadIdx.x; b < B_; b += 1024)
-        s += lq[b] - lpz[b] + bacc[b] - lpx[b] + lkl[b];
-    #pragma unroll
-    for (int off = 32; off; off >>= 1) s += __shfl_down(s, off);
-    int wave = threadIdx.x >> 6, lane = threadIdx.x & 63;
-    if (lane == 0) red[wave] = s;
-    __syncthreads();
-    if (threadIdx.x == 0) {
-        float t = 0.0f;
-        for (int i = 0; i < 16; ++i) t += red[i];
-        out[0] = t / (float)B_;
-    }
 }
 
 extern "C" void kernel_launch(void* const* d_in, const int* in_sizes, int n_in,
@@ -713,8 +821,8 @@
         return r;
     };
     _Float16* xh    = (_Float16*)alloc((size_t)B_ * X_ * 2);
-    _Float16* zha   = (_Float16*)alloc((size_t)B_ * H_ * 2);
-    _Float16* zhb   = (_Float16*)alloc((size_t)B_ * H_ * 2);
+    _Float16* zb0   = (_Float16*)alloc((size_t)B_ * H_ * 2);
+    _Float16* zb1   = (_Float16*)alloc((size_t)B_ * H_ * 2);
     _Float16* lath  = (_Float16*)alloc((size_t)B_ * Z_ * 2);
     _Float16* Wf1h  = (_Float16*)alloc((size_t)H_ * X_ * 2);
     _Float16* eWihh = (_Float16*)alloc((size_t)L_ * G3_ * X_ * 2);
@@ -730,10 +838,7 @@
     float* eWihc  = (float*)alloc((size_t)L_ * G3_ * 4);
     float* dWihc  = (float*)alloc((size_t)L_ * G3_ * 4);
     float* z      = (float*)alloc((size_t)B_ * H_ * 4);
-    float* dbuf   = (float*)alloc((size_t)B_ * H_ * 4);
-    float* latent = (float*)alloc((size_t)B_ * Z_ * 4);
     float* wt     = (float*)alloc((size_t)L_ * B_ * W_ * 4);
-    float* logits = (float*)alloc((size_t)B_ * X_ * 4);
     float* lq     = (float*)alloc((size_t)B_ * 4);
     float* lpz    = (float*)alloc((size_t)B_ * 4);
     float* lpx    = (float*)alloc((size_t)B_ * 4);
@@ -741,7 +846,6 @@
     float* bacc   = (float*)alloc((size_t)B_ * 4);
 
     const dim3 blk(256);
-    const int nBH = B_ * H_;
     auto cgrid = [](long total) { return dim3((unsigned)((total / 8 + 255) / 256)); };
 
     ConvJobs J;
@@ -761,54 +865,26 @@
     stack_bias<<<1, 128, 0, stream>>>(bmu, blv, bml);
     extract_col<<<(L_ * G3_ + 255) / 256, blk, 0, stream>>>(eWih, eWihc, X_ + 1, X_, L_ * G3_);
     extract_col<<<(L_ * G3_ + 255) / 256, blk, 0, stream>>>(dWih, dWihc, Z_ + 1, Z_, L_ * G3_);
-    wtrans<<<(W_ * B_) / 256, blk, 0, stream>>>(workers, wt, bacc);
-
-    predict_head<X_><<<B_ / 32, blk, 0, stream>>>(xh, Wf1h, bf1, Wf2, bf2, t, L_);
-
-    _Float16* zcur = zha;
-    _Float16* znxt = zhb;
-    for (int l = 0; l < L_; ++l) {
-        if (l == 0)
-            gru_fused<1, X_, 1><<<512, blk, 0, stream>>>(
-                xh, eWihh, ebih, eWhhh, ebhh, eWihc, t, enc_eps, zcur, z, znxt);
-        else
-            gru_fused<1, X_, 0><<<512, blk, 0, stream>>>(
-                xh, eWihh + (long)l * G3_ * X_, ebih + (long)l * G3_,
-                eWhhh + (long)l * G3_ * H_, ebhh + (long)l * G3_,
-                eWihc + (long)l * G3_, t + l, enc_eps + (long)l * nBH,
-                zcur, z, znxt);
-        _Float16* tmp = zcur; zcur = znxt; znxt = tmp;
-        if (l < L_ - 1)
-            predict_head<H_><<<B_ / 32, blk, 0, stream>>>(
-                zcur, eWdh + (long)l * H_ * H_, ebd + (long)l * H_,
-                eWo + (long)l * H_, ebo + l, t + (l + 1), L_);
-    }
-
-    mfma_gemm<64><<<dim3(2, B_ / 128), blk, 0, stream>>>(
-        zcur, Wmlh, bml, dbuf, 128, H_, 0);
-    latent_elem<<<B_ / 4, blk, 0, stream>>>(dbuf, samp_eps, latent, lath, lq, lpz);
-
-    zcur = zha; znxt = zhb;
-    for (int l = 0; l < L_; ++l) {
-        if (l == 0)
-            gru_fused<2, Z_, 1><<<512, blk, 0, stream>>>(
-                lath, dWihh, dbih, dWhhh, dbhh, dWihc, t, dec_eps, zcur, z, znxt);
-        else
-            gru_fused<2, Z_, 0><<<512, blk, 0, stream>>>(
-                lath, dWihh + (long)l * G3_ * Z_, dbih + (long)l * G3_,
-                dWhhh + (long)l * G3_ * H_, dbhh + (long)l * G3_,
-                dWihc + (long)l * G3_, t + l, dec_eps + (long)l * nBH,
-                zcur, z, znxt);
-        _Float16* tmp = zcur; zcur = znxt; znxt = tmp;
-        dec_head_bce<<<B_ / 32, blk, 0, stream>>>(
-            zcur, dWdh + (long)l * H_ * H_, dbd + (long)l * H_,
-            dWoh + (long)l * W_ * H_, dbo + (long)l * W_,
-            wt + (long)l * B_ * W_, bacc);
-    }
-
-    mfma_gemm<128><<<dim3(X_ / 128, B_ / 128), blk, 0, stream>>>(
-        zcur, Wrh, br, logits, X_, H_, 0);
-    logpx_reduce<<<B_ / 4, blk, 0, stream>>>(logits, x, lpx);
-    kl_kernel<<<B_ / 256, blk, 0, stream>>>(t, workers, lkl);
-    final_reduce<<<1, 1024, 0, stream>>>(lq, lpz, bacc, lpx, lkl, loss);
-}
+    wtrans<<<(W_ * B_) / 256, blk, 0, stream>>>(workers, wt, bacc, lpx);
+
+    EncP ep;
+    ep.xh = xh; ep.Wf1h = Wf1h; ep.eWihh = eWihh; ep.eWhhh = eWhhh; ep.eWdh = eWdh;
+    ep.bf1 = bf1; ep.Wf2 = Wf2; ep.bf2 = bf2; ep.ebih = ebih; ep.ebhh = ebhh;
+    ep.eWihc = eWihc; ep.ebd = ebd; ep.eWo = eWo; ep.ebo = ebo;
+    ep.enc_eps = enc_eps; ep.workers = workers;
+    ep.t = t; ep.z = z; ep.lkl = lkl; ep.zb0 = zb0; ep.zb1 = zb1;
+    void* ea[] = { (void*)&ep };
+    hipLaunchCooperativeKernel((void*)enc_scan, dim3(256), dim3(512), ea, 0, stream);
+
+    DecP dp;
+    dp.zfin = zb0; dp.Wmlh = Wmlh; dp.dWihh = dWihh; dp.dWhhh = dWhhh;
+    dp.dWdh = dWdh; dp.dWoh = dWoh; dp.Wrh = Wrh;
+    dp.bml = bml; dp.samp_eps = samp_eps; dp.dbih = dbih; dp.dbhh = dbhh;
+    dp.dWihc = dWihc; dp.dbd = dbd; dp.dbo = dbo; dp.br = br; dp.x = x; dp.wtr = wt;
+    dp.t = t; dp.dec_eps = dec_eps;
+    dp.lath = lath; dp.zb0 = zb0; dp.zb1 = zb1;
+    dp.z = z; dp.lq = lq; dp.lpz = lpz; dp.bacc = bacc; dp.lpx = lpx;
+    dp.lkl = lkl; dp.loss = loss;
+    void* da[] = { (void*)&dp };
+    hipLaunchCooperativeKernel((void*)dec_scan, dim3(256), dim3(512), da, 0, stream);
+}
```

Measured after the change: 2.516 ms. 2.27x slower.
